# Kernel optimization log

Hardware: AMD Instinct MI355X
Metric: run time of the kernel (lower is better)

Reference implementation:

```python
import jax, jax.numpy as jnp
import numpy as np
from jax import lax

S_IN = 16; V_IN = 16; S_OUT = 16; V_OUT = 16
SIZE = 7; STRIDE = 2; PAD = 3; EPS = 1e-5
# n_basis per (rep_out, rep_in) pair = n_radial(3) * number of allowed CG paths
NB = {('s','s'): 3, ('s','v'): 3, ('s','t'): 9, ('v','s'): 3, ('v','v'): 9, ('v','t'): 21}
DIMS = {'s': 1, 'v': 3, 't': 9}  # repr1, repr3, repr3x3 dimensions


def _basis(key, nb, d_out, d_in):
    # Stand-in for the constant steerable basis (spherical harmonics x Clebsch-Gordan
    # x radial windows). These are data-independent constants in se3cnn; the compute
    # pattern (weighted basis sum -> dense 3D conv) is identical.
    return jax.random.normal(key, (nb, d_out, d_in, SIZE, SIZE, SIZE), jnp.float32) / np.sqrt(SIZE ** 3)


def setup_inputs() -> dict:
    key = jax.random.key(0)
    ks = jax.random.split(key, 16)
    inp = {"sv": jax.random.normal(ks[0], (4, S_IN + 3 * V_IN, 32, 32, 32), jnp.float32)}
    mul_in = {'s': S_IN, 'v': V_IN, 't': V_IN}
    i = 1
    for o in ['s', 'v']:
        mo = S_OUT if o == 's' else V_OUT
        for a in ['s', 'v', 't']:
            nb = NB[(o, a)]
            inp[f"basis_{o}{a}"] = _basis(ks[i], nb, DIMS[o], DIMS[a])
            inp[f"w_{o}{a}"] = jax.random.normal(ks[i + 1], (mo, mul_in[a], nb), jnp.float32) / np.sqrt(nb * mul_in[a] * DIMS[a])
            i += 2
    inp["bn_g_s"] = jnp.ones((S_OUT,), jnp.float32)
    inp["bn_g_v"] = jnp.ones((V_OUT,), jnp.float32)
    inp["bias_s"] = jnp.zeros((S_OUT,), jnp.float32)
    return inp


def _block(w, basis):
    # w: [mul_out, mul_in, nb], basis: [nb, d_out, d_in, 7,7,7] -> [mul_out*d_out, mul_in*d_in, 7,7,7]
    mo, mi, nb = w.shape
    do, di = basis.shape[1], basis.shape[2]
    k = jnp.einsum('uvb,bijxyz->uivjxyz', w, basis)
    return k.reshape(mo * do, mi * di, SIZE, SIZE, SIZE)


def _forward(sv, w_ss, w_sv, w_st, w_vs, w_vv, w_vt,
             basis_ss, basis_sv, basis_st, basis_vs, basis_vv, basis_vt,
             bn_g_s, bn_g_v, bias_s):
    B = sv.shape[0]; sp = sv.shape[2:]
    # TensorProduct: vector fields -> vector (x) vector = repr3x3 (9 channels each)
    v = sv[:, S_IN:].reshape(B, V_IN, 3, *sp)
    t = jnp.einsum('buixyz,bujxyz->buijxyz', v, v).reshape(B, V_IN * 9, *sp)
    svt = jnp.concatenate([sv, t], axis=1)  # [B, S_IN + 3*V_IN + 9*V_IN, X,Y,Z]
    # SE3Convolution: assemble kernel from steerable basis, then dense 3D conv
    row_s = jnp.concatenate([_block(w_ss, basis_ss), _block(w_sv, basis_sv), _block(w_st, basis_st)], axis=1)
    row_v = jnp.concatenate([_block(w_vs, basis_vs), _block(w_vv, basis_vv), _block(w_vt, basis_vt)], axis=1)
    kernel = jnp.concatenate([row_s, row_v], axis=0)  # [S_OUT + 3*V_OUT, 208, 7,7,7]
    y = lax.conv_general_dilated(svt, kernel, (STRIDE,) * 3, [(PAD, PAD)] * 3,
                                 dimension_numbers=('NCDHW', 'OIDHW', 'NCDHW'))
    osp = y.shape[2:]
    # SE3BatchNorm: per-field second-moment normalization (training-mode batch stats)
    ys = y[:, :S_OUT]
    yv = y[:, S_OUT:].reshape(B, V_OUT, 3, *osp)
    var_s = jnp.mean(ys * ys, axis=(0, 2, 3, 4))
    ys = ys * (bn_g_s / jnp.sqrt(var_s + EPS))[None, :, None, None, None]
    var_v = jnp.mean(yv * yv, axis=(0, 2, 3, 4, 5))
    yv = yv * (bn_g_v / jnp.sqrt(var_v + EPS))[None, :, None, None, None, None]
    # BiasRelu: bias + relu on scalar fields only; vector fields pass through
    ys = jax.nn.relu(ys + bias_s[None, :, None, None, None])
    return jnp.concatenate([ys, yv.reshape(B, 3 * V_OUT, *osp)], axis=1)


def reference(sv, w_ss, w_sv, w_st, w_vs, w_vv, w_vt,
              basis_ss, basis_sv, basis_st, basis_vs, basis_vv, basis_vt,
              bn_g_s, bn_g_v, bias_s):
    return _forward(sv, w_ss, w_sv, w_st, w_vs, w_vv, w_vt,
                    basis_ss, basis_sv, basis_st, basis_vs, basis_vv, basis_vt,
                    bn_g_s, bn_g_v, bias_s)
```

## Files before the change

kernel.cpp:

```cpp
#include <hip/hip_runtime.h>
#include <hip/hip_bf16.h>


using f4  = __attribute__((ext_vector_type(4)))  float;
using f16v= __attribute__((ext_vector_type(16))) float;
using s8  = __attribute__((ext_vector_type(8)))  short;

#define C_TOT 160
#define PZ_   37
#define NTAP  343
#define NROW  (4 * PZ_ * PZ_)
#define KSN   16
#define NT5   490
#define SLICE_E 1048576

#define AROW    1232
#define B_OFF   20480
#define LDS_SZ  (B_OFF + 14336)

__device__ __forceinline__ void gl_lds16(const void* g, void* l) {
    __builtin_amdgcn_global_load_lds(
        (const __attribute__((address_space(1))) unsigned int*)g,
        (__attribute__((address_space(3))) unsigned int*)l, 16, 0, 0);
}

__device__ __forceinline__ void pair_ij(int p, int& i, int& j) {
    if (p < 3)      { i = p; j = p; }
    else if (p == 3){ i = 0; j = 1; }
    else if (p == 4){ i = 0; j = 2; }
    else            { i = 1; j = 2; }
}

struct bf2 { __hip_bfloat16 x, y; };
struct bh4 { __hip_bfloat16 x, y, z, w; };

__global__ void prep_kernel(
    const float* __restrict__ sv,
    const float* __restrict__ b_ss, const float* __restrict__ w_ss,
    const float* __restrict__ b_sv, const float* __restrict__ w_sv,
    const float* __restrict__ b_st, const float* __restrict__ w_st,
    const float* __restrict__ b_vs, const float* __restrict__ w_vs,
    const float* __restrict__ b_vv, const float* __restrict__ w_vv,
    const float* __restrict__ b_vt, const float* __restrict__ w_vt,
    __hip_bfloat16* __restrict__ xt, __hip_bfloat16* __restrict__ wl)
{
    __shared__ float S[13056];
    const int tid = threadIdx.x;

    if (blockIdx.x < 1372) {
        float* L = S;
        float* W = S + 768;
        const int tap = blockIdx.x >> 2;
        const int jq  = (blockIdx.x & 3) * 10;
        for (int r = tid; r < 750; r += 256) {
            float v;
            if (r < 3)        v = b_ss[r * NTAP + tap];
            else if (r < 12)  v = b_sv[(r - 3) * NTAP + tap];
            else if (r < 93)  v = b_st[(r - 12) * NTAP + tap];
            else if (r < 102) v = b_vs[(r - 93) * NTAP + tap];
            else if (r < 183) v = b_vv[(r - 102) * NTAP + tap];
            else              v = b_vt[(r - 183) * NTAP + tap];
            L[r] = v;
        }
        for (int r = tid; r < 12288; r += 256) {
            float v;
            if (r < 768)       v = w_ss[r];
            else if (r < 1536) v = w_sv[r - 768];
            else if (r < 3840) v = w_st[r - 1536];
            else if (r < 4608) v = w_vs[r - 3840];
            else if (r < 6912) v = w_vv[r - 4608];
            else               v = w_vt[r - 6912];
            W[r] = v;
        }
        __syncthreads();
        for (int j = jq; j < jq + 10; ++j) {
            const int idx = j * 256 + tid;
            const int c = idx % C_TOT, n = idx / C_TOT;
            float acc = 0.f;
            if (n < 16) {
                const int u = n;
                if (c < 16) {
                    for (int t = 0; t < 3; ++t) acc += W[(u*16 + c)*3 + t] * L[t];
                } else if (c < 64) {
                    int mm = (c-16)/3, di = (c-16)%3;
                    for (int t = 0; t < 3; ++t)
                        acc += W[768 + (u*16+mm)*3 + t] * L[3 + t*3 + di];
                } else {
                    int q = c-64, mm = q/6, p = q%6, i, jj;
                    pair_ij(p, i, jj);
                    int d1 = i*3+jj, d2 = jj*3+i;
                    for (int t = 0; t < 9; ++t) {
                        float bs = L[12 + t*9 + d1];
                        if (i != jj) bs += L[12 + t*9 + d2];
                        acc += W[1536 + (u*16+mm)*9 + t] * bs;
                    }
                }
            } else {
                const int u = (n-16)/3, dn = (n-16)%3;
                if (c < 16) {
                    for (int t = 0; t < 3; ++t)
                        acc += W[3840 + (u*16+c)*3 + t] * L[93 + t*3 + dn];
                } else if (c < 64) {
                    int mm = (c-16)/3, di = (c-16)%3;
                    for (int t = 0; t < 9; ++t)
                        acc += W[4608 + (u*16+mm)*9 + t] * L[102 + (t*3+dn)*3 + di];
                } else {
                    int q = c-64, mm = q/6, p = q%6, i, jj;
                    pair_ij(p, i, jj);
                    int d1 = i*3+jj, d2 = jj*3+i;
                    for (int t = 0; t < 21; ++t) {
                        float bs = L[183 + (t*3+dn)*9 + d1];
                        if (i != jj) bs += L[183 + (t*3+dn)*9 + d2];
                        acc += W[6912 + (u*16+mm)*21 + t] * bs;
                    }
                }
            }
            const int chunk = c >> 4, cw = c & 15;
            wl[((size_t)chunk * NTAP + tap) * 1024 + (size_t)n * 16 + cw] =
                __float2bfloat16(acc);
        }
    } else {
        float* row = S;
        const int bid = blockIdx.x - 1372;
        const int y = bid % 37, z = (bid / 37) % 37, b = bid / 1369;
        const bool interior = (z >= 3 && z < 35 && y >= 3 && y < 35);
        if (interior) {
            const float* src = sv + (size_t)b * 2097152 + (z-3) * 1024 + (y-3) * 32;
            for (int f = tid; f < 2048; f += 256) {
                int ch = f >> 5, x = f & 31;
                row[x * 66 + ch] = src[(size_t)ch * 32768 + x];
            }
        }
        __syncthreads();
        for (int e2 = tid; e2 < 38 * 80; e2 += 256) {
            const int s = e2 / 80, cp = e2 % 80, c = cp * 2;
            float v0 = 0.f, v1 = 0.f;
            if (interior && s >= 3 && s < 35) {
                const int x = s - 3;
                if (c < 64) {
                    v0 = row[x * 66 + c];
                    v1 = row[x * 66 + c + 1];
                } else {
                    int q = c - 64, u = q / 6, p = q % 6, i, j;
                    pair_ij(p, i, j);
                    v0 = row[x * 66 + 16 + u * 3 + i] * row[x * 66 + 16 + u * 3 + j];
                    pair_ij(p + 1, i, j);
                    v1 = row[x * 66 + 16 + u * 3 + i] * row[x * 66 + 16 + u * 3 + j];
                }
            }
            bf2 w{__float2bfloat16(v0), __float2bfloat16(v1)};
            const int chunk = c >> 4, cw = c & 15;
            *(bf2*)(xt + ((size_t)chunk * NROW + bid) * 608 + s * 16 + cw) = w;
        }
    }
}

__global__ __launch_bounds__(256, 4) void conv_mfma_kernel(
    const __hip_bfloat16* __restrict__ xt,
    const __hip_bfloat16* __restrict__ wl,
    __hip_bfloat16* __restrict__ y4b)
{
    __shared__ __align__(16) char lds[LDS_SZ];

    const int phys = blockIdx.x;
    const int bid  = (phys & 7) * (64 * KSN / 8) + (phys >> 3);

    const int low3 = bid & 7;
    const int rest = bid >> 3;
    const int ks   = rest % KSN;
    const int mb   = (rest / KSN) * 8 + low3;
    const int b    = mb >> 4;
    const int oz0 = ((mb >> 2) & 3) * 4;
    const int oy0 = (mb & 3) * 4;

    const int tid  = threadIdx.x;
    const int w    = tid >> 6;
    const int lane = tid & 63;
    const int m    = lane & 31;
    const int h    = lane >> 5;

    int  invA[5];  char* dstA[5];
#pragma unroll
    for (int k = 0; k < 5; ++k) {
        const int i = w + 4 * k;
        const int o = i * 1024 + lane * 16;
        int r = o / AROW;
        int rem = o - r * AROW;
        if (r > 15) { r = 15; rem = 0; }
        if (rem >= 1216) rem = 0;
        const int s  = rem >> 5;
        const int cg = ((rem >> 4) & 1) ^ ((s >> 1) & 1);
        const int base_row = (b * PZ_ + 2 * (oz0 + (r >> 2))) * PZ_
                           + 2 * (oy0 + (r & 3));
        invA[k] = base_row * 608 + s * 16 + cg * 8;
        dstA[k] = lds + i * 1024;
    }
    int  invB[4];  char* dstB[4];  int nB = 0;
#pragma unroll
    for (int k = 0; k < 4; ++k) {
        const int i = w + 4 * k;
        if (i < 14) {
            const int kx = i >> 1, nt = i & 1;
            invB[k] = kx * 1024 + (nt * 32 + m) * 16 + h * 8;
            dstB[k] = lds + B_OFF + i * 1024;
            nB = k + 1;
        }
    }

    f16v acc[2][2];
    for (int t = 0; t < 2; ++t)
        for (int n = 0; n < 2; ++n)
            for (int k = 0; k < 16; ++k) acc[t][n][k] = 0.f;

    const int rA0   = ((m >> 4) << 2) + ((m >> 2) & 3);
    const int sbase = (w << 3) + ((m & 3) << 1);

    for (int t5 = ks; t5 < NT5; t5 += KSN) {
        const int chunk = t5 / 49;
        const int zy    = t5 - chunk * 49;
        const int kz = zy / 7, ky = zy - kz * 7;
        const int u_a = (chunk * NROW + kz * PZ_ + ky) * 608;
        const int u_b = (chunk * NTAP + zy * 7) * 1024;
        __syncthreads();

#pragma unroll
        for (int k = 0; k < 5; ++k)
            gl_lds16(xt + u_a + invA[k], dstA[k]);
#pragma unroll
        for (int k = 0; k < 4; ++k)
            if (k < nB) gl_lds16(wl + u_b + invB[k], dstB[k]);
        __syncthreads();

#pragma unroll
        for (int kx = 0; kx < 7; ++kx) {
            const int s   = sbase + kx;
            const int cgp = h ^ ((s >> 1) & 1);
            const char* ap = lds + rA0 * AROW + s * 32 + cgp * 16;
            const s8 a0 = *(const s8*)(ap);
            const s8 a1 = *(const s8*)(ap + 8 * AROW);
            const char* bp = lds + B_OFF + kx * 2048 + h * 512 + m * 16;
            const s8 b0 = *(const s8*)(bp);
            const s8 b1 = *(const s8*)(bp + 1024);
            acc[0][0] = __builtin_amdgcn_mfma_f32_32x32x16_bf16(a0, b0, acc[0][0], 0, 0, 0);
            acc[0][1] = __builtin_amdgcn_mfma_f32_32x32x16_bf16(a0, b1, acc[0][1], 0, 0, 0);
            acc[1][0] = __builtin_amdgcn_mfma_f32_32x32x16_bf16(a1, b0, acc[1][0], 0, 0, 0);
            acc[1][1] = __builtin_amdgcn_mfma_f32_32x32x16_bf16(a1, b1, acc[1][1], 0, 0, 0);
        }
    }

    const int nl = lane & 31;
    f4* yb = (f4*)lds;
    __hip_bfloat16* dst0 = y4b + (size_t)ks * SLICE_E + (size_t)(b * 64) * 4096;
#pragma unroll
    for (int t = 0; t < 2; ++t) {
        __syncthreads();
#pragma unroll
        for (int nt = 0; nt < 2; ++nt) {
            const int n = nt * 32 + nl;
#pragma unroll
            for (int q = 0; q < 4; ++q) {
                const int rr = 2 * q + h;
                f4 v = { acc[t][nt][4*q], acc[t][nt][4*q+1],
                         acc[t][nt][4*q+2], acc[t][nt][4*q+3] };
                yb[n * 33 + rr * 4 + w] = v;
            }
        }
        __syncthreads();
        for (int j = tid; j < 2048; j += 256) {
            const int n  = j >> 5, sp = j & 31;
            f4 v = yb[n * 33 + sp];
            const int rr = sp >> 2, wq = sp & 3;
            const int my = rr & 3, mz = t * 2 + (rr >> 2);
            bh4 p{__float2bfloat16(v.x), __float2bfloat16(v.y),
                  __float2bfloat16(v.z), __float2bfloat16(v.w)};
            *(bh4*)(dst0 + (size_t)n * 4096 +
                    (oz0 + mz) * 256 + (oy0 + my) * 16 + wq * 4) = p;
        }
    }
}

__global__ void combine_reduce_kernel(const __hip_bfloat16* __restrict__ y4b,
                                      float* __restrict__ yc,
                                      float* __restrict__ sums2)
{
    const int n = blockIdx.x & 63, q = blockIdx.x >> 6;
    const size_t base = ((size_t)q * 64 + n) * 4096;
    float s = 0.f;
    for (int i = threadIdx.x; i < 1024; i += 256) {
        const size_t off = base + (size_t)i * 4;
        f4 v = {0.f, 0.f, 0.f, 0.f};
#pragma unroll
        for (int k = 0; k < KSN; ++k) {
            bh4 r = *(const bh4*)(y4b + off + (size_t)k * SLICE_E);
            v.x += (float)r.x; v.y += (float)r.y;
            v.z += (float)r.z; v.w += (float)r.w;
        }
        *(f4*)(yc + off) = v;
        s += v.x * v.x + v.y * v.y + v.z * v.z + v.w * v.w;
    }
    __shared__ float red[256];
    red[threadIdx.x] = s;
    __syncthreads();
    for (int st = 128; st > 0; st >>= 1) {
        if (threadIdx.x < st) red[threadIdx.x] += red[threadIdx.x + st];
        __syncthreads();
    }
    if (threadIdx.x == 0) sums2[n * 4 + q] = red[0];
}

__global__ void finalize_kernel(const float* __restrict__ yc,
                                const float* __restrict__ sums2,
                                const float* __restrict__ g_s,
                                const float* __restrict__ g_v,
                                const float* __restrict__ bias_s,
                                float* __restrict__ out)
{
    const int idx = blockIdx.x * 256 + threadIdx.x;
    const int n = (idx >> 12) & 63;
    float v = yc[idx];
    if (n < 16) {
        float sum = sums2[n*4] + sums2[n*4+1] + sums2[n*4+2] + sums2[n*4+3];
        float var = sum * (1.0f / 16384.0f);
        float sc  = g_s[n] / sqrtf(var + 1e-5f);
        v = fmaxf(v * sc + bias_s[n], 0.f);
    } else {
        int u = (n - 16) / 3;
        float sum = 0.f;
        for (int k = 0; k < 12; ++k) sum += sums2[(16 + u * 3) * 4 + k];
        float var = sum * (1.0f / 49152.0f);
        v = v * (g_v[u] / sqrtf(var + 1e-5f));
    }
    out[idx] = v;
}

extern "C" void kernel_launch(void* const* d_in, const int* in_sizes, int n_in,
                              void* d_out, int out_size, void* d_ws, size_t ws_size,
                              hipStream_t stream)
{
    const float* sv    = (const float*)d_in[0];
    const float* b_ss  = (const float*)d_in[1];
    const float* w_ss  = (const float*)d_in[2];
    const float* b_sv  = (const float*)d_in[3];
    const float* w_sv  = (const float*)d_in[4];
    const float* b_st  = (const float*)d_in[5];
    const float* w_st  = (const float*)d_in[6];
    const float* b_vs  = (const float*)d_in[7];
    const float* w_vs  = (const float*)d_in[8];
    const float* b_vv  = (const float*)d_in[9];
    const float* w_vv  = (const float*)d_in[10];
    const float* b_vt  = (const float*)d_in[11];
    const float* w_vt  = (const float*)d_in[12];
    const float* bn_gs = (const float*)d_in[13];
    const float* bn_gv = (const float*)d_in[14];
    const float* bias_s= (const float*)d_in[15];
    float* out = (float*)d_out;

    char* ws = (char*)d_ws;
    constexpr size_t XT_BYTES = (size_t)10 * NROW * 1216;
    constexpr size_t WL_BYTES = (size_t)10 * NTAP * 2048;
    constexpr size_t Y4_BYTES = (size_t)KSN * SLICE_E * 2;
    constexpr size_t YC_BYTES = (size_t)4 * 64 * 4096 * 4;

    __hip_bfloat16* xt  = (__hip_bfloat16*)ws;
    __hip_bfloat16* wl  = (__hip_bfloat16*)(ws + XT_BYTES);
    __hip_bfloat16* y4b = (__hip_bfloat16*)(ws + XT_BYTES + WL_BYTES);
    float* yc    = (float*)(ws + XT_BYTES + WL_BYTES + Y4_BYTES);
    float* sums2 = (float*)(ws + XT_BYTES + WL_BYTES + Y4_BYTES + YC_BYTES);

    prep_kernel<<<1372 + 5476, 256, 0, stream>>>(
        sv, b_ss, w_ss, b_sv, w_sv, b_st, w_st, b_vs, w_vs, b_vv, w_vv,
        b_vt, w_vt, xt, wl);
    conv_mfma_kernel<<<64 * KSN, 256, 0, stream>>>(xt, wl, y4b);
    combine_reduce_kernel<<<256, 256, 0, stream>>>(y4b, yc, sums2);
    finalize_kernel<<<4096, 256, 0, stream>>>(yc, sums2, bn_gs, bn_gv, bias_s, out);
}
```

Measured before the change: 285.3 us.

## Double-buffer LDS tiles in conv MFMA loop and halve split-K slices

The conv kernel's main loop now double-buffers its LDS tiles. The global-to-LDS loads for the next tap step are issued before the MFMA work on the current buffer, so each iteration needs one barrier instead of two and load latency can overlap with compute. LDS use doubles, so launch bounds drop to 2 blocks per SM, and the split-K factor KSN is halved from 16 to 8. That gives fewer blocks with longer K loops and less partial-sum output, at the cost of lower occupancy and less grid-level parallelism.

```diff
diff --git a/kernel.cpp b/kernel.cpp
--- a/kernel.cpp
+++ b/kernel.cpp
@@ -10,13 +10,14 @@
 #define PZ_   37
 #define NTAP  343
 #define NROW  (4 * PZ_ * PZ_)
-#define KSN   16
+#define KSN   8
 #define NT5   490
 #define SLICE_E 1048576
 
 #define AROW    1232
 #define B_OFF   20480
-#define LDS_SZ  (B_OFF + 14336)
+#define BUFSZ   34816
+#define LDS_SZ  (2 * BUFSZ)
 
 __device__ __forceinline__ void gl_lds16(const void* g, void* l) {
     __builtin_amdgcn_global_load_lds(
@@ -155,7 +156,7 @@
     }
 }
 
-__global__ __launch_bounds__(256, 4) void conv_mfma_kernel(
+__global__ __launch_bounds__(256, 2) void conv_mfma_kernel(
     const __hip_bfloat16* __restrict__ xt,
     const __hip_bfloat16* __restrict__ wl,
     __hip_bfloat16* __restrict__ y4b)
@@ -179,7 +180,7 @@
     const int m    = lane & 31;
     const int h    = lane >> 5;
 
-    int  invA[5];  char* dstA[5];
+    int invA[5], offA[5];
 #pragma unroll
     for (int k = 0; k < 5; ++k) {
         const int i = w + 4 * k;
@@ -193,16 +194,16 @@
         const int base_row = (b * PZ_ + 2 * (oz0 + (r >> 2))) * PZ_
                            + 2 * (oy0 + (r & 3));
         invA[k] = base_row * 608 + s * 16 + cg * 8;
-        dstA[k] = lds + i * 1024;
-    }
-    int  invB[4];  char* dstB[4];  int nB = 0;
+        offA[k] = i * 1024;
+    }
+    int invB[4], offB[4];  int nB = 0;
 #pragma unroll
     for (int k = 0; k < 4; ++k) {
         const int i = w + 4 * k;
         if (i < 14) {
             const int kx = i >> 1, nt = i & 1;
             invB[k] = kx * 1024 + (nt * 32 + m) * 16 + h * 8;
-            dstB[k] = lds + B_OFF + i * 1024;
+            offB[k] = B_OFF + i * 1024;
             nB = k + 1;
         }
     }
@@ -215,30 +216,29 @@
     const int rA0   = ((m >> 4) << 2) + ((m >> 2) & 3);
     const int sbase = (w << 3) + ((m & 3) << 1);
 
-    for (int t5 = ks; t5 < NT5; t5 += KSN) {
-        const int chunk = t5 / 49;
-        const int zy    = t5 - chunk * 49;
+    auto stage = [&](int t5s, int bufofs) {
+        const int chunk = t5s / 49;
+        const int zy    = t5s - chunk * 49;
         const int kz = zy / 7, ky = zy - kz * 7;
         const int u_a = (chunk * NROW + kz * PZ_ + ky) * 608;
         const int u_b = (chunk * NTAP + zy * 7) * 1024;
-        __syncthreads();
-
 #pragma unroll
         for (int k = 0; k < 5; ++k)
-            gl_lds16(xt + u_a + invA[k], dstA[k]);
+            gl_lds16(xt + u_a + invA[k], lds + bufofs + offA[k]);
 #pragma unroll
         for (int k = 0; k < 4; ++k)
-            if (k < nB) gl_lds16(wl + u_b + invB[k], dstB[k]);
-        __syncthreads();
-
+            if (k < nB) gl_lds16(wl + u_b + invB[k], lds + bufofs + offB[k]);
+    };
+
+    auto compute = [&](int bufofs) {
 #pragma unroll
         for (int kx = 0; kx < 7; ++kx) {
             const int s   = sbase + kx;
             const int cgp = h ^ ((s >> 1) & 1);
-            const char* ap = lds + rA0 * AROW + s * 32 + cgp * 16;
+            const char* ap = lds + bufofs + rA0 * AROW + s * 32 + cgp * 16;
             const s8 a0 = *(const s8*)(ap);
             const s8 a1 = *(const s8*)(ap + 8 * AROW);
-            const char* bp = lds + B_OFF + kx * 2048 + h * 512 + m * 16;
+            const char* bp = lds + bufofs + B_OFF + kx * 2048 + h * 512 + m * 16;
             const s8 b0 = *(const s8*)(bp);
             const s8 b1 = *(const s8*)(bp + 1024);
             acc[0][0] = __builtin_amdgcn_mfma_f32_32x32x16_bf16(a0, b0, acc[0][0], 0, 0, 0);
@@ -246,6 +246,21 @@
             acc[1][0] = __builtin_amdgcn_mfma_f32_32x32x16_bf16(a1, b0, acc[1][0], 0, 0, 0);
             acc[1][1] = __builtin_amdgcn_mfma_f32_32x32x16_bf16(a1, b1, acc[1][1], 0, 0, 0);
         }
+    };
+
+    stage(ks, 0);
+    __syncthreads();
+    int buf = 0;
+    int t5  = ks;
+    for (;;) {
+        const int t5n = t5 + KSN;
+        const bool more = (t5n < NT5);
+        if (more) stage(t5n, buf ^ BUFSZ);
+        compute(buf);
+        if (!more) break;
+        __syncthreads();
+        buf ^= BUFSZ;
+        t5 = t5n;
     }
 
     const int nl = lane & 31;
```

Measured after the change: 275.7 us. 3.4% less time.

## Reuse staged input rows across ky taps and double-buffer weight tiles

Applied to the files above, without the earlier changes.

Each block now covers a full oz slice of 16 output y-rows. It stages the even and odd padded input rows once per (chunk,kz) group and reuses them across all seven ky taps, where before it reloaded A for every tap. Weight tiles are double-buffered so the next tap's B load overlaps the current MFMA work, and the K split drops from 16 to 8, which halves the partial-sum slices. LDS use roughly doubles and launch bounds drop to 2 blocks per CU, which lowers occupancy. Work per block becomes uneven (9 vs 8 groups).

```diff
diff --git a/kernel.cpp b/kernel.cpp
--- a/kernel.cpp
+++ b/kernel.cpp
@@ -10,13 +10,18 @@
 #define PZ_   37
 #define NTAP  343
 #define NROW  (4 * PZ_ * PZ_)
-#define KSN   16
-#define NT5   490
+#define KSN   8
 #define SLICE_E 1048576
 
 #define AROW    1232
-#define B_OFF   20480
-#define LDS_SZ  (B_OFF + 14336)
+#define AE_ROWS 19
+#define AO_ROWS 18
+#define AE_SZ   23552
+#define AO_OFF  23552
+#define AO_SZ   22528
+#define B_OFF   46080
+#define BSZ     14336
+#define LDS_SZ  (B_OFF + 2 * BSZ)
 
 __device__ __forceinline__ void gl_lds16(const void* g, void* l) {
     __builtin_amdgcn_global_load_lds(
@@ -155,7 +160,7 @@
     }
 }
 
-__global__ __launch_bounds__(256, 4) void conv_mfma_kernel(
+__global__ __launch_bounds__(256, 2) void conv_mfma_kernel(
     const __hip_bfloat16* __restrict__ xt,
     const __hip_bfloat16* __restrict__ wl,
     __hip_bfloat16* __restrict__ y4b)
@@ -170,8 +175,7 @@
     const int ks   = rest % KSN;
     const int mb   = (rest / KSN) * 8 + low3;
     const int b    = mb >> 4;
-    const int oz0 = ((mb >> 2) & 3) * 4;
-    const int oy0 = (mb & 3) * 4;
+    const int oz   = mb & 15;
 
     const int tid  = threadIdx.x;
     const int w    = tid >> 6;
@@ -179,30 +183,45 @@
     const int m    = lane & 31;
     const int h    = lane >> 5;
 
-    int  invA[5];  char* dstA[5];
-#pragma unroll
-    for (int k = 0; k < 5; ++k) {
+    int invAE[6]; int nAE = 0;
+#pragma unroll
+    for (int k = 0; k < 6; ++k) {
         const int i = w + 4 * k;
-        const int o = i * 1024 + lane * 16;
-        int r = o / AROW;
-        int rem = o - r * AROW;
-        if (r > 15) { r = 15; rem = 0; }
-        if (rem >= 1216) rem = 0;
-        const int s  = rem >> 5;
-        const int cg = ((rem >> 4) & 1) ^ ((s >> 1) & 1);
-        const int base_row = (b * PZ_ + 2 * (oz0 + (r >> 2))) * PZ_
-                           + 2 * (oy0 + (r & 3));
-        invA[k] = base_row * 608 + s * 16 + cg * 8;
-        dstA[k] = lds + i * 1024;
-    }
-    int  invB[4];  char* dstB[4];  int nB = 0;
+        if (i < 23) {
+            const int o = i * 1024 + lane * 16;
+            int r = o / AROW;
+            int rem = o - r * AROW;
+            if (r > AE_ROWS - 1) { r = AE_ROWS - 1; rem = 0; }
+            if (rem >= 1216) rem = 0;
+            const int s  = rem >> 5;
+            const int cg = ((rem >> 4) & 1) ^ ((s >> 1) & 1);
+            invAE[k] = (2 * r) * 608 + s * 16 + cg * 8;
+            nAE = k + 1;
+        }
+    }
+    int invAO[6]; int nAO = 0;
+#pragma unroll
+    for (int k = 0; k < 6; ++k) {
+        const int i = w + 4 * k;
+        if (i < 22) {
+            const int o = i * 1024 + lane * 16;
+            int r = o / AROW;
+            int rem = o - r * AROW;
+            if (r > AO_ROWS - 1) { r = AO_ROWS - 1; rem = 0; }
+            if (rem >= 1216) rem = 0;
+            const int s  = rem >> 5;
+            const int cg = ((rem >> 4) & 1) ^ ((s >> 1) & 1);
+            invAO[k] = (2 * r + 1) * 608 + s * 16 + cg * 8;
+            nAO = k + 1;
+        }
+    }
+    int invB[4]; int nB = 0;
 #pragma unroll
     for (int k = 0; k < 4; ++k) {
         const int i = w + 4 * k;
         if (i < 14) {
             const int kx = i >> 1, nt = i & 1;
             invB[k] = kx * 1024 + (nt * 32 + m) * 16 + h * 8;
-            dstB[k] = lds + B_OFF + i * 1024;
             nB = k + 1;
         }
     }
@@ -215,30 +234,41 @@
     const int rA0   = ((m >> 4) << 2) + ((m >> 2) & 3);
     const int sbase = (w << 3) + ((m & 3) << 1);
 
-    for (int t5 = ks; t5 < NT5; t5 += KSN) {
-        const int chunk = t5 / 49;
-        const int zy    = t5 - chunk * 49;
-        const int kz = zy / 7, ky = zy - kz * 7;
-        const int u_a = (chunk * NROW + kz * PZ_ + ky) * 608;
-        const int u_b = (chunk * NTAP + zy * 7) * 1024;
-        __syncthreads();
-
-#pragma unroll
-        for (int k = 0; k < 5; ++k)
-            gl_lds16(xt + u_a + invA[k], dstA[k]);
+    auto stageAE = [&](int g) {
+        const int chunk = g / 7, kz = g - chunk * 7;
+        const size_t u = ((size_t)chunk * NROW + (size_t)(b * PZ_ + 2 * oz + kz) * PZ_) * 608;
+#pragma unroll
+        for (int k = 0; k < 6; ++k)
+            if (k < nAE) gl_lds16(xt + u + invAE[k], lds + (w + 4 * k) * 1024);
+    };
+    auto stageAO = [&](int g) {
+        const int chunk = g / 7, kz = g - chunk * 7;
+        const size_t u = ((size_t)chunk * NROW + (size_t)(b * PZ_ + 2 * oz + kz) * PZ_) * 608;
+#pragma unroll
+        for (int k = 0; k < 6; ++k)
+            if (k < nAO) gl_lds16(xt + u + invAO[k], lds + AO_OFF + (w + 4 * k) * 1024);
+    };
+    auto stageB = [&](int g, int kyv, int bsel) {
+        const int chunk = g / 7, kz = g - chunk * 7;
+        const size_t u = ((size_t)chunk * NTAP + (size_t)(kz * 7 + kyv) * 7) * 1024;
+        char* dst = lds + B_OFF + bsel * BSZ;
 #pragma unroll
         for (int k = 0; k < 4; ++k)
-            if (k < nB) gl_lds16(wl + u_b + invB[k], dstB[k]);
-        __syncthreads();
-
+            if (k < nB) gl_lds16(wl + u + invB[k], dst + (w + 4 * k) * 1024);
+    };
+
+    auto compute = [&](int ky, int bsel) {
+        const int abase = (ky & 1) ? AO_OFF : 0;
+        const char* abp = lds + abase + (rA0 + (ky >> 1)) * AROW;
+        const char* bbp = lds + B_OFF + bsel * BSZ;
 #pragma unroll
         for (int kx = 0; kx < 7; ++kx) {
             const int s   = sbase + kx;
             const int cgp = h ^ ((s >> 1) & 1);
-            const char* ap = lds + rA0 * AROW + s * 32 + cgp * 16;
+            const char* ap = abp + s * 32 + cgp * 16;
             const s8 a0 = *(const s8*)(ap);
             const s8 a1 = *(const s8*)(ap + 8 * AROW);
-            const char* bp = lds + B_OFF + kx * 2048 + h * 512 + m * 16;
+            const char* bp = bbp + kx * 2048 + h * 512 + m * 16;
             const s8 b0 = *(const s8*)(bp);
             const s8 b1 = *(const s8*)(bp + 1024);
             acc[0][0] = __builtin_amdgcn_mfma_f32_32x32x16_bf16(a0, b0, acc[0][0], 0, 0, 0);
@@ -246,11 +276,35 @@
             acc[1][0] = __builtin_amdgcn_mfma_f32_32x32x16_bf16(a1, b0, acc[1][0], 0, 0, 0);
             acc[1][1] = __builtin_amdgcn_mfma_f32_32x32x16_bf16(a1, b1, acc[1][1], 0, 0, 0);
         }
+    };
+
+    const int G = (ks < 6) ? 9 : 8;
+    const int T = G * 7;
+    stageAO(ks);
+    stageB(ks, 1, 0);
+    __syncthreads();
+    int bB = 0;
+    for (int t = 0; t < T; ++t) {
+        const int gi = t / 7, p = t - gi * 7;
+        const int g  = ks + gi * KSN;
+        const int ky = (p < 3) ? (2 * p + 1) : (2 * (p - 3));
+        const int tn = t + 1;
+        if (tn < T) {
+            const int gin = tn / 7, pn = tn - gin * 7;
+            const int kyn = (pn < 3) ? (2 * pn + 1) : (2 * (pn - 3));
+            stageB(ks + gin * KSN, kyn, bB ^ 1);
+        }
+        if (p == 0) stageAE(g);
+        else if (p == 3 && g + KSN < 70) stageAO(g + KSN);
+        compute(ky, bB);
+        __syncthreads();
+        bB ^= 1;
     }
 
     const int nl = lane & 31;
     f4* yb = (f4*)lds;
-    __hip_bfloat16* dst0 = y4b + (size_t)ks * SLICE_E + (size_t)(b * 64) * 4096;
+    __hip_bfloat16* dst0 = y4b + (size_t)ks * SLICE_E + (size_t)(b * 64) * 4096
+                         + (size_t)oz * 256;
 #pragma unroll
     for (int t = 0; t < 2; ++t) {
         __syncthreads();
@@ -270,11 +324,10 @@
             const int n  = j >> 5, sp = j & 31;
             f4 v = yb[n * 33 + sp];
             const int rr = sp >> 2, wq = sp & 3;
-            const int my = rr & 3, mz = t * 2 + (rr >> 2);
+            const int yo = t * 8 + (rr >> 2) * 4 + (rr & 3);
             bh4 p{__float2bfloat16(v.x), __float2bfloat16(v.y),
                   __float2bfloat16(v.z), __float2bfloat16(v.w)};
-            *(bh4*)(dst0 + (size_t)n * 4096 +
-                    (oz0 + mz) * 256 + (oy0 + my) * 16 + wq * 4) = p;
+            *(bh4*)(dst0 + (size_t)n * 4096 + yo * 16 + wq * 4) = p;
         }
     }
 }
```

After: 275.4 us. 1.04x faster.
